# Kernel tuning notes

Measured on AMD Instinct MI355X. Metric: run time of the kernel, lower is better.

Reference implementation:

```python
import jax, jax.numpy as jnp
from jax import lax
import numpy as np

EPS = 1e-5
ALPHA = 0.2  # LeakyReLU slope


def setup_inputs() -> dict:
    key = jax.random.key(0)
    ks = jax.random.split(key, 8)
    B, N, F_IN, HID, OUT, H = 32, 512, 256, 512, 512, 4
    D = OUT // H
    return {
        "x": jax.random.normal(ks[0], (B, N, F_IN), dtype=jnp.float32),
        "adj": jax.random.uniform(ks[1], (N, N), dtype=jnp.float32),
        "gc_w": jax.random.normal(ks[2], (F_IN, HID), dtype=jnp.float32) * 0.04,
        "gc_b": jax.random.normal(ks[3], (HID,), dtype=jnp.float32) * 0.04,
        "bn1_g": jnp.ones((HID,), jnp.float32),
        "bn1_b": jnp.zeros((HID,), jnp.float32),
        "bn1_m": jnp.zeros((HID,), jnp.float32),
        "bn1_v": jnp.ones((HID,), jnp.float32),
        "gat_w": jax.random.normal(ks[4], (H, D, HID), dtype=jnp.float32) * 0.04,
        "conv_w": jax.random.normal(ks[5], (OUT, OUT, 3), dtype=jnp.float32) * 0.02,
        "conv_b": jax.random.normal(ks[6], (OUT,), dtype=jnp.float32) * 0.02,
        "bn2_g": jnp.ones((OUT,), jnp.float32),
        "bn2_b": jnp.zeros((OUT,), jnp.float32),
        "bn2_m": jnp.zeros((OUT,), jnp.float32),
        "bn2_v": jnp.ones((OUT,), jnp.float32),
    }


def reference(x, adj, gc_w, gc_b, bn1_g, bn1_b, bn1_m, bn1_v, gat_w,
              conv_w, conv_b, bn2_g, bn2_b, bn2_m, bn2_v):
    # --- GraphConvolution: adj @ (x @ W) + b ---
    support = jnp.einsum('bnc,cd->bnd', x, gc_w)
    g = jnp.einsum('nm,bmd->bnd', adj, support) + gc_b  # [B,N,HID]
    # --- BatchNorm1d over channel dim (eval mode) + ReLU ---
    g = (g - bn1_m) * (bn1_g / jnp.sqrt(bn1_v + EPS)) + bn1_b
    g = jax.nn.relu(g)
    # --- Multi-head GAT (repeat/mul/sum == attention-weighted matmul) ---
    hh = jnp.einsum('bnf,hdf->bhnd', g, gat_w)           # per-head projections
    e = jnp.einsum('bhnd,bhmd->bhnm', hh, hh)            # logits [B,H,N,N]
    e = jnp.where(e > 0, e, ALPHA * e)                   # LeakyReLU
    att = jax.nn.softmax(e, axis=-1)
    o = jnp.einsum('bhnm,bhmd->bhnd', att, hh)
    B, H, N, D = o.shape
    o = o.transpose(0, 2, 1, 3).reshape(B, N, H * D)     # concat heads [B,N,OUT]
    # --- TCN block: conv1d(k=3,pad=1) over node axis + BN(eval) + ReLU ---
    xc = o.transpose(0, 2, 1)                            # [B,C,N]
    y = lax.conv_general_dilated(xc, conv_w, (1,), ((1, 1),),
                                 dimension_numbers=('NCH', 'OIH', 'NCH'))
    y = y + conv_b[None, :, None]
    y = (y - bn2_m[None, :, None]) * (bn2_g / jnp.sqrt(bn2_v + EPS))[None, :, None] + bn2_b[None, :, None]
    y = jax.nn.relu(y)
    return y.transpose(0, 2, 1)                          # [B,N,OUT]
```

## Files before the change

kernel.cpp:

```cpp
#include <hip/hip_runtime.h>
#include <math.h>

#define BATCH 32
#define NNODE 512
#define FIN   256
#define HIDC  512
#define OUTC  512
#define NHEAD 4
#define HDIM  128
#define EPSV  1e-5f
#define ALPHA_LR 0.2f

typedef _Float16 half8 __attribute__((ext_vector_type(8)));
typedef _Float16 half4v __attribute__((ext_vector_type(4)));
typedef float floatx4 __attribute__((ext_vector_type(4)));

#define GLOBAL_TO_LDS16(g, l)                                                  \
  __builtin_amdgcn_global_load_lds(                                            \
      (const __attribute__((address_space(1))) void*)(g),                      \
      (__attribute__((address_space(3))) void*)(l), 16, 0, 0)

__device__ __forceinline__ void split_gemm_acc(
    const _Float16* __restrict__ Ah, const _Float16* __restrict__ Al, int lda,
    const _Float16* __restrict__ Bh, const _Float16* __restrict__ Bl, int ldb,
    int K, int rowBase, int colBase,
    _Float16* sAh, _Float16* sAl, _Float16* sBh, _Float16* sBl,
    floatx4 acc[4][4], int tid) {
  const int lane = tid & 63, wave = tid >> 6;
  const int wr = (wave >> 1) * 64, wc = (wave & 1) * 64;
  const int fr = lane & 15, q = lane >> 4;
  const int r = tid >> 2, ko = (tid & 3) * 8;
  for (int k0 = 0; k0 < K; k0 += 32) {
    GLOBAL_TO_LDS16(&Ah[(size_t)(rowBase + r) * lda + k0 + ko], &sAh[tid * 8]);
    GLOBAL_TO_LDS16(&Ah[(size_t)(rowBase + r + 64) * lda + k0 + ko], &sAh[2048 + tid * 8]);
    GLOBAL_TO_LDS16(&Al[(size_t)(rowBase + r) * lda + k0 + ko], &sAl[tid * 8]);
    GLOBAL_TO_LDS16(&Al[(size_t)(rowBase + r + 64) * lda + k0 + ko], &sAl[2048 + tid * 8]);
    GLOBAL_TO_LDS16(&Bh[(size_t)(colBase + r) * ldb + k0 + ko], &sBh[tid * 8]);
    GLOBAL_TO_LDS16(&Bh[(size_t)(colBase + r + 64) * ldb + k0 + ko], &sBh[2048 + tid * 8]);
    GLOBAL_TO_LDS16(&Bl[(size_t)(colBase + r) * ldb + k0 + ko], &sBl[tid * 8]);
    GLOBAL_TO_LDS16(&Bl[(size_t)(colBase + r + 64) * ldb + k0 + ko], &sBl[2048 + tid * 8]);
    __syncthreads();
    half8 ah[4], al4[4], bh[4], bl4[4];
#pragma unroll
    for (int i = 0; i < 4; ++i) {
      ah[i]  = *(const half8*)&sAh[(wr + i * 16 + fr) * 32 + q * 8];
      al4[i] = *(const half8*)&sAl[(wr + i * 16 + fr) * 32 + q * 8];
    }
#pragma unroll
    for (int j = 0; j < 4; ++j) {
      bh[j]  = *(const half8*)&sBh[(wc + j * 16 + fr) * 32 + q * 8];
      bl4[j] = *(const half8*)&sBl[(wc + j * 16 + fr) * 32 + q * 8];
    }
#pragma unroll
    for (int i = 0; i < 4; ++i)
#pragma unroll
      for (int j = 0; j < 4; ++j) {
        acc[i][j] = __builtin_amdgcn_mfma_f32_16x16x32_f16(al4[i], bh[j], acc[i][j], 0, 0, 0);
        acc[i][j] = __builtin_amdgcn_mfma_f32_16x16x32_f16(ah[i], bl4[j], acc[i][j], 0, 0, 0);
        acc[i][j] = __builtin_amdgcn_mfma_f32_16x16x32_f16(ah[i], bh[j], acc[i][j], 0, 0, 0);
      }
    __syncthreads();
  }
}

__global__ __launch_bounds__(256) void k_prep(
    const float* __restrict__ adj, const float* __restrict__ gcw,
    const float* __restrict__ gatw, const float* __restrict__ cw,
    const float* __restrict__ X,
    _Float16* __restrict__ ADJh, _Float16* __restrict__ ADJl,
    _Float16* __restrict__ GWh, _Float16* __restrict__ GWl,
    _Float16* __restrict__ GAh, _Float16* __restrict__ GAl,
    _Float16* __restrict__ WT, _Float16* __restrict__ OP,
    _Float16* __restrict__ Xh, _Float16* __restrict__ Xl) {
  const int i = blockIdx.x * 256 + threadIdx.x;
  if (i < 262144) {
    float v = adj[i];
    _Float16 h = (_Float16)v;
    ADJh[i] = h; ADJl[i] = (_Float16)(v - (float)h);
  } else if (i < 393216) {
    int j = i - 262144;
    int n = j >> 8, k = j & 255;
    float v = gcw[(size_t)k * HIDC + n];
    _Float16 h = (_Float16)v;
    GWh[j] = h; GWl[j] = (_Float16)(v - (float)h);
  } else if (i < 655360) {
    int j = i - 393216;
    float v = gatw[j];
    _Float16 h = (_Float16)v;
    GAh[j] = h; GAl[j] = (_Float16)(v - (float)h);
  } else if (i < 1441792) {
    int j = i - 655360;
    int n = j / 1536, kk = j - n * 1536;
    int tap = kk >> 9, ci = kk & 511;
    WT[j] = (_Float16)cw[(size_t)n * 1536 + ci * 3 + tap];
  } else if (i < 1474560) {
    int j = i - 1441792;
    int b = j >> 10, rs = (j >> 9) & 1, c = j & 511;
    OP[((size_t)b * 514 + rs * 513) * OUTC + c] = (_Float16)0.f;
  } else if (i < 2523136) {
    int j = (i - 1474560) * 4;
    float4 v = *(const float4*)&X[j];
    half4v h, l;
    h[0] = (_Float16)v.x; l[0] = (_Float16)(v.x - (float)h[0]);
    h[1] = (_Float16)v.y; l[1] = (_Float16)(v.y - (float)h[1]);
    h[2] = (_Float16)v.z; l[2] = (_Float16)(v.z - (float)h[2]);
    h[3] = (_Float16)v.w; l[3] = (_Float16)(v.w - (float)h[3]);
    *(half4v*)&Xh[j] = h;
    *(half4v*)&Xl[j] = l;
  }
}

__global__ __launch_bounds__(256) void k_support_t(
    const _Float16* __restrict__ GWh, const _Float16* __restrict__ GWl,
    const _Float16* __restrict__ Xh, const _Float16* __restrict__ Xl,
    _Float16* __restrict__ STh, _Float16* __restrict__ STl) {
  __shared__ _Float16 sm[4][4096];
  const int tid = threadIdx.x;
  const int rowBase = blockIdx.y * 128, colBase = blockIdx.x * 128;
  floatx4 acc[4][4] = {};
  split_gemm_acc(GWh, GWl, FIN, Xh, Xl, FIN, FIN, rowBase, colBase,
                 sm[0], sm[1], sm[2], sm[3], acc, tid);
  const int lane = tid & 63, wave = tid >> 6;
  const int wr = (wave >> 1) * 64, wc = (wave & 1) * 64;
  const int fr = lane & 15, q = lane >> 4;
#pragma unroll
  for (int i = 0; i < 4; ++i) {
    const int ch0 = rowBase + wr + i * 16 + q * 4;
#pragma unroll
    for (int rg = 0; rg < 4; ++rg) {
      size_t base = (size_t)(ch0 + rg) * 16384 + colBase + wc + fr;
#pragma unroll
      for (int j = 0; j < 4; ++j) {
        float v = acc[i][j][rg];
        _Float16 h = (_Float16)v;
        STh[base + j * 16] = h;
        STl[base + j * 16] = (_Float16)(v - (float)h);
      }
    }
  }
}

__global__ __launch_bounds__(256) void k_gcn(
    const _Float16* __restrict__ ADJh, const _Float16* __restrict__ ADJl,
    const _Float16* __restrict__ STh, const _Float16* __restrict__ STl,
    const float* __restrict__ gcb, const float* __restrict__ g1,
    const float* __restrict__ b1, const float* __restrict__ m1,
    const float* __restrict__ v1,
    _Float16* __restrict__ Gh, _Float16* __restrict__ Gl) {
  __shared__ _Float16 sm[4][4096];
  const int tid = threadIdx.x;
  const int rowBase = blockIdx.y * 128, colBase = blockIdx.x * 128;
  const int b = blockIdx.z;
  floatx4 acc[4][4] = {};
  split_gemm_acc(ADJh, ADJl, NNODE, STh + (size_t)b * NNODE, STl + (size_t)b * NNODE,
                 16384, NNODE, rowBase, colBase, sm[0], sm[1], sm[2], sm[3], acc, tid);
  const int lane = tid & 63, wave = tid >> 6;
  const int wr = (wave >> 1) * 64, wc = (wave & 1) * 64;
  const int fr = lane & 15, q = lane >> 4;
  float sc[4], of[4];
#pragma unroll
  for (int j = 0; j < 4; ++j) {
    int c = colBase + wc + j * 16 + fr;
    float s = g1[c] * rsqrtf(v1[c] + EPSV);
    sc[j] = s;
    of[j] = (gcb[c] - m1[c]) * s + b1[c];
  }
#pragma unroll
  for (int i = 0; i < 4; ++i) {
    const int n0 = rowBase + wr + i * 16 + q * 4;
#pragma unroll
    for (int rg = 0; rg < 4; ++rg) {
      size_t base = ((size_t)b * NNODE + n0 + rg) * HIDC + colBase + wc + fr;
#pragma unroll
      for (int j = 0; j < 4; ++j) {
        float v = fmaxf(fmaf(acc[i][j][rg], sc[j], of[j]), 0.0f);
        _Float16 h = (_Float16)v;
        Gh[base + j * 16] = h;
        Gl[base + j * 16] = (_Float16)(v - (float)h);
      }
    }
  }
}

__global__ __launch_bounds__(256) void k_hh(
    const _Float16* __restrict__ Gh, const _Float16* __restrict__ Gl,
    const _Float16* __restrict__ GAh, const _Float16* __restrict__ GAl,
    _Float16* __restrict__ HHh, _Float16* __restrict__ HHl) {
  __shared__ _Float16 sm[4][4096];
  const int tid = threadIdx.x;
  const int rowBase = blockIdx.y * 128, colBase = blockIdx.x * 128;
  floatx4 acc[4][4] = {};
  split_gemm_acc(Gh, Gl, HIDC, GAh, GAl, HIDC, HIDC, rowBase, colBase,
                 sm[0], sm[1], sm[2], sm[3], acc, tid);
  const int lane = tid & 63, wave = tid >> 6;
  const int wr = (wave >> 1) * 64, wc = (wave & 1) * 64;
  const int fr = lane & 15, q = lane >> 4;
#pragma unroll
  for (int i = 0; i < 4; ++i) {
    const int r0 = rowBase + wr + i * 16 + q * 4;
#pragma unroll
    for (int rg = 0; rg < 4; ++rg) {
      size_t base = (size_t)(r0 + rg) * OUTC + colBase + wc + fr;
#pragma unroll
      for (int j = 0; j < 4; ++j) {
        float v = acc[i][j][rg];
        _Float16 h = (_Float16)v;
        HHh[base + j * 16] = h;
        HHl[base + j * 16] = (_Float16)(v - (float)h);
      }
    }
  }
}

__global__ __launch_bounds__(256) void k_vt(const _Float16* __restrict__ HHh,
                                            _Float16* __restrict__ HHT) {
  __shared__ _Float16 sT[128 * 132];
  const int bt = blockIdx.x;
  const int nt = bt & 3, g = bt >> 2;
  const int bb = g >> 2, h = g & 3;
  const int tid = threadIdx.x;
  const int rr = tid >> 4, cc = (tid & 15) * 8;
#pragma unroll
  for (int it = 0; it < 8; ++it) {
    int node = rr + it * 16;
    half8 v = *(const half8*)&HHh[((size_t)bb * 512 + nt * 128 + node) * 512 + h * 128 + cc];
#pragma unroll
    for (int e = 0; e < 8; ++e) sT[(cc + e) * 132 + node] = v[e];
  }
  __syncthreads();
#pragma unroll
  for (int it = 0; it < 8; ++it) {
    int d = rr + it * 16;
    half8 v;
#pragma unroll
    for (int e = 0; e < 8; ++e) v[e] = sT[d * 132 + cc + e];
    *(half8*)&HHT[((size_t)g * 128 + d) * 512 + nt * 128 + cc] = v;
  }
}

__global__ __launch_bounds__(256, 4) void k_attn(
    const _Float16* __restrict__ HHh, const _Float16* __restrict__ HHl,
    const _Float16* __restrict__ HHT, _Float16* __restrict__ OP) {
  __shared__ _Float16 sK[8][2048];
  _Float16* sV = &sK[0][0];
  _Float16* sP = &sK[4][0];
  const int tid = threadIdx.x;
  const int lane = tid & 63, wave = tid >> 6;
  const int fr = lane & 15, q = lane >> 4;
  const int id = blockIdx.x;
  const int slot = id >> 3;
  const int g = (id & 7) + 8 * (slot >> 3);
  const int qBase = (slot & 7) * 64;
  const int bb = g >> 2, h = g & 3;
  const int w16 = wave * 16;
  const _Float16* Qh = HHh + (size_t)bb * NNODE * OUTC + h * HDIM;
  const _Float16* Ql = HHl + (size_t)bb * NNODE * OUTC + h * HDIM;
  const _Float16* VT = HHT + (size_t)g * HDIM * NNODE;
  const int rk = tid >> 2, ck = (tid & 3) * 8;

  half8 qh[4], ql[4];
#pragma unroll
  for (int k0 = 0; k0 < 4; ++k0) {
    const size_t off = (size_t)(qBase + w16 + fr) * OUTC + k0 * 32 + q * 8;
    qh[k0] = *(const half8*)&Qh[off];
    ql[k0] = *(const half8*)&Ql[off];
  }

  floatx4 oacc[8] = {};
  float m_i[4], l_i[4];
#pragma unroll
  for (int rg = 0; rg < 4; ++rg) { m_i[rg] = -1e30f; l_i[rg] = 0.f; }

  for (int kt = 0; kt < 8; ++kt) {
    const int ktb = kt * 64;
#pragma unroll
    for (int t = 0; t < 4; ++t) {
      GLOBAL_TO_LDS16(&Qh[(size_t)(ktb + rk) * OUTC + t * 32 + ck], &sK[t][tid * 8]);
      GLOBAL_TO_LDS16(&Ql[(size_t)(ktb + rk) * OUTC + t * 32 + ck], &sK[4 + t][tid * 8]);
    }
    __syncthreads();
    floatx4 sacc[4] = {};
#pragma unroll
    for (int k0 = 0; k0 < 4; ++k0)
#pragma unroll
      for (int j = 0; j < 4; ++j) {
        half8 bh = *(const half8*)&sK[k0][(j * 16 + fr) * 32 + q * 8];
        half8 bl = *(const half8*)&sK[4 + k0][(j * 16 + fr) * 32 + q * 8];
        sacc[j] = __builtin_amdgcn_mfma_f32_16x16x32_f16(ql[k0], bh, sacc[j], 0, 0, 0);
        sacc[j] = __builtin_amdgcn_mfma_f32_16x16x32_f16(qh[k0], bl, sacc[j], 0, 0, 0);
        sacc[j] = __builtin_amdgcn_mfma_f32_16x16x32_f16(qh[k0], bh, sacc[j], 0, 0, 0);
      }
    __syncthreads();
#pragma unroll
    for (int j = 0; j < 4; ++j)
#pragma unroll
      for (int rg = 0; rg < 4; ++rg) {
        float v = sacc[j][rg];
        sacc[j][rg] = v > 0.f ? v : ALPHA_LR * v;
      }
#pragma unroll
    for (int rg = 0; rg < 4; ++rg) {
      float mx = sacc[0][rg];
#pragma unroll
      for (int j = 1; j < 4; ++j) mx = fmaxf(mx, sacc[j][rg]);
      mx = fmaxf(mx, __shfl_xor(mx, 1));
      mx = fmaxf(mx, __shfl_xor(mx, 2));
      mx = fmaxf(mx, __shfl_xor(mx, 4));
      mx = fmaxf(mx, __shfl_xor(mx, 8));
      float mnew = fmaxf(m_i[rg], mx);
      float alpha = __expf(m_i[rg] - mnew);
      m_i[rg] = mnew;
      float sum = 0.f;
#pragma unroll
      for (int j = 0; j < 4; ++j) {
        float p = __expf(sacc[j][rg] - mnew);
        sacc[j][rg] = p;
        sum += p;
      }
      sum += __shfl_xor(sum, 1);
      sum += __shfl_xor(sum, 2);
      sum += __shfl_xor(sum, 4);
      sum += __shfl_xor(sum, 8);
      l_i[rg] = l_i[rg] * alpha + sum;
#pragma unroll
      for (int j = 0; j < 8; ++j) oacc[j][rg] *= alpha;
    }
#pragma unroll
    for (int l = 0; l < 4; ++l)
      GLOBAL_TO_LDS16(&VT[(size_t)((l >> 1) * 64 + rk) * NNODE + ktb + (l & 1) * 32 + ck],
                      &sV[(l & 1) * 4096 + (l >> 1) * 2048 + tid * 8]);
#pragma unroll
    for (int j = 0; j < 4; ++j)
#pragma unroll
      for (int rg = 0; rg < 4; ++rg)
        sP[(w16 + q * 4 + rg) * 68 + j * 16 + fr] = (_Float16)sacc[j][rg];
    __syncthreads();
#pragma unroll
    for (int ks = 0; ks < 2; ++ks) {
      half8 pa = *(const half8*)&sP[(w16 + fr) * 68 + ks * 32 + q * 8];
#pragma unroll
      for (int j = 0; j < 8; ++j) {
        half8 bv = *(const half8*)&sV[ks * 4096 + (j * 16 + fr) * 32 + q * 8];
        oacc[j] = __builtin_amdgcn_mfma_f32_16x16x32_f16(pa, bv, oacc[j], 0, 0, 0);
      }
    }
    __syncthreads();
  }
#pragma unroll
  for (int rg = 0; rg < 4; ++rg) {
    const float inv = 1.0f / l_i[rg];
    const int node = qBase + w16 + q * 4 + rg;
    size_t base = ((size_t)bb * 514 + 1 + node) * OUTC + h * HDIM + fr;
#pragma unroll
    for (int j = 0; j < 8; ++j)
      OP[base + j * 16] = (_Float16)(oacc[j][rg] * inv);
  }
}

__global__ __launch_bounds__(256) void k_conv_mfma(
    const _Float16* __restrict__ OP, const _Float16* __restrict__ WT,
    const float* __restrict__ cb, const float* __restrict__ g2,
    const float* __restrict__ b2, const float* __restrict__ m2,
    const float* __restrict__ v2, float* __restrict__ Y) {
  __shared__ _Float16 At[128 * 32];
  __shared__ _Float16 Bt[128 * 32];
  const int tid = threadIdx.x;
  const int lane = tid & 63, wave = tid >> 6;
  const int wr = (wave >> 1) * 64, wc = (wave & 1) * 64;
  const int id = blockIdx.y * 4 + blockIdx.x;
  const int jj = id >> 3;
  const int rowBase = ((id & 7) * 16 + (jj >> 2)) * 128;
  const int colBase = (jj & 3) * 128;
  const int b = rowBase >> 9;
  const int n0 = rowBase & 511;
  const int r = tid >> 2;
  const int ko = (tid & 3) * 8;
  floatx4 acc[4][4] = {};
  for (int k0 = 0; k0 < 3 * OUTC; k0 += 32) {
    const int tap = k0 >> 9;
    const int cib = k0 & 511;
    const size_t abase = ((size_t)b * 514 + n0 + tap) * OUTC + cib + ko;
    GLOBAL_TO_LDS16(&OP[abase + (size_t)r * OUTC],        &At[tid * 8]);
    GLOBAL_TO_LDS16(&OP[abase + (size_t)(r + 64) * OUTC], &At[2048 + tid * 8]);
    GLOBAL_TO_LDS16(&WT[(size_t)(colBase + r) * 1536 + k0 + ko],      &Bt[tid * 8]);
    GLOBAL_TO_LDS16(&WT[(size_t)(colBase + r + 64) * 1536 + k0 + ko], &Bt[2048 + tid * 8]);
    __syncthreads();
    const int fr = lane & 15, q = lane >> 4;
    half8 af[4], bf[4];
#pragma unroll
    for (int i = 0; i < 4; ++i)
      af[i] = *(const half8*)&At[(wr + i * 16 + fr) * 32 + q * 8];
#pragma unroll
    for (int j = 0; j < 4; ++j)
      bf[j] = *(const half8*)&Bt[(wc + j * 16 + fr) * 32 + q * 8];
#pragma unroll
    for (int i = 0; i < 4; ++i)
#pragma unroll
      for (int j = 0; j < 4; ++j)
        acc[i][j] = __builtin_amdgcn_mfma_f32_16x16x32_f16(af[i], bf[j], acc[i][j], 0, 0, 0);
    __syncthreads();
  }
  const int fr = lane & 15, q = lane >> 4;
  float sc[4], of[4];
#pragma unroll
  for (int j = 0; j < 4; ++j) {
    int c = colBase + wc + j * 16 + fr;
    float s = g2[c] * rsqrtf(v2[c] + EPSV);
    sc[j] = s;
    of[j] = (cb[c] - m2[c]) * s + b2[c];
  }
#pragma unroll
  for (int i = 0; i < 4; ++i) {
    const int R0r = rowBase + wr + i * 16 + q * 4;
#pragma unroll
    for (int rg = 0; rg < 4; ++rg) {
      float* dst = &Y[(size_t)(R0r + rg) * OUTC + colBase + wc + fr];
#pragma unroll
      for (int j = 0; j < 4; ++j)
        dst[j * 16] = fmaxf(fmaf(acc[i][j][rg], sc[j], of[j]), 0.0f);
    }
  }
}

extern "C" void kernel_launch(void* const* d_in, const int* in_sizes, int n_in,
                              void* d_out, int out_size, void* d_ws, size_t ws_size,
                              hipStream_t stream) {
  const float* x     = (const float*)d_in[0];
  const float* adj   = (const float*)d_in[1];
  const float* gc_w  = (const float*)d_in[2];
  const float* gc_b  = (const float*)d_in[3];
  const float* bn1_g = (const float*)d_in[4];
  const float* bn1_b = (const float*)d_in[5];
  const float* bn1_m = (const float*)d_in[6];
  const float* bn1_v = (const float*)d_in[7];
  const float* gat_w = (const float*)d_in[8];
  const float* conv_w= (const float*)d_in[9];
  const float* conv_b= (const float*)d_in[10];
  const float* bn2_g = (const float*)d_in[11];
  const float* bn2_b = (const float*)d_in[12];
  const float* bn2_m = (const float*)d_in[13];
  const float* bn2_v = (const float*)d_in[14];
  float* out = (float*)d_out;

  char* ws = (char*)d_ws;
  _Float16* STh = (_Float16*)(ws + 0);
  _Float16* STl = (_Float16*)(ws + 16777216);
  _Float16* HHh = (_Float16*)(ws + 0);
  _Float16* HHl = (_Float16*)(ws + 16777216);
  _Float16* Xh  = (_Float16*)(ws + 33554432);
  _Float16* Xl  = (_Float16*)(ws + 41943040);
  _Float16* Gh  = (_Float16*)(ws + 33554432);
  _Float16* Gl  = (_Float16*)(ws + 50331648);
  _Float16* HHT = (_Float16*)(ws + 33554432);
  _Float16* OP  = (_Float16*)(ws + 67108864);
  _Float16* WT  = (_Float16*)(ws + 83951616);
  _Float16* ADJh= (_Float16*)(ws + 85524480);
  _Float16* ADJl= (_Float16*)(ws + 86048768);
  _Float16* GWh = (_Float16*)(ws + 86573056);
  _Float16* GWl = (_Float16*)(ws + 86835200);
  _Float16* GAh = (_Float16*)(ws + 87097344);
  _Float16* GAl = (_Float16*)(ws + 87621632);

  k_prep<<<9856, 256, 0, stream>>>(adj, gc_w, gat_w, conv_w, x,
                                   ADJh, ADJl, GWh, GWl, GAh, GAl, WT, OP, Xh, Xl);
  k_support_t<<<dim3(128, 4), 256, 0, stream>>>(GWh, GWl, Xh, Xl, STh, STl);
  k_gcn<<<dim3(4, 4, 32), 256, 0, stream>>>(ADJh, ADJl, STh, STl, gc_b,
                                            bn1_g, bn1_b, bn1_m, bn1_v, Gh, Gl);
  k_hh<<<dim3(4, 128), 256, 0, stream>>>(Gh, Gl, GAh, GAl, HHh, HHl);
  k_vt<<<512, 256, 0, stream>>>(HHh, HHT);
  k_attn<<<1024, 256, 0, stream>>>(HHh, HHl, HHT, OP);
  k_conv_mfma<<<dim3(4, 128), 256, 0, stream>>>(OP, WT, conv_b,
                                                bn2_g, bn2_b, bn2_m, bn2_v, out);
}
```

Measured before the change: 303.8 us.

## Prefetch next key tile into ping-pong LDS halves during attention softmax

The attention kernel now keeps a 32KB LDS buffer split into alternating hi/lo halves plus a separate P buffer. The next key tile's high part is issued during the softmax and PV stages, overlapping it with compute, and the low part is loaded after PV into the freed half. This cuts one barrier-exposed load per iteration but raises LDS use, so launch bounds drop from 4 to 3 blocks per CU, which may lower occupancy. The V tile is also issued earlier, right after the QK stage.

```diff
diff --git a/kernel.cpp b/kernel.cpp
--- a/kernel.cpp
+++ b/kernel.cpp
@@ -238,12 +238,11 @@
   }
 }
 
-__global__ __launch_bounds__(256, 4) void k_attn(
+__global__ __launch_bounds__(256, 3) void k_attn(
     const _Float16* __restrict__ HHh, const _Float16* __restrict__ HHl,
     const _Float16* __restrict__ HHT, _Float16* __restrict__ OP) {
-  __shared__ _Float16 sK[8][2048];
-  _Float16* sV = &sK[0][0];
-  _Float16* sP = &sK[4][0];
+  __shared__ _Float16 sK[16384];
+  __shared__ _Float16 sP[64 * 68];
   const int tid = threadIdx.x;
   const int lane = tid & 63, wave = tid >> 6;
   const int fr = lane & 15, q = lane >> 4;
@@ -271,26 +270,39 @@
 #pragma unroll
   for (int rg = 0; rg < 4; ++rg) { m_i[rg] = -1e30f; l_i[rg] = 0.f; }
 
+#pragma unroll
+  for (int t = 0; t < 4; ++t) {
+    GLOBAL_TO_LDS16(&Qh[(size_t)rk * OUTC + t * 32 + ck], &sK[t * 2048 + tid * 8]);
+    GLOBAL_TO_LDS16(&Ql[(size_t)rk * OUTC + t * 32 + ck], &sK[8192 + t * 2048 + tid * 8]);
+  }
+  __syncthreads();
+
   for (int kt = 0; kt < 8; ++kt) {
     const int ktb = kt * 64;
-#pragma unroll
-    for (int t = 0; t < 4; ++t) {
-      GLOBAL_TO_LDS16(&Qh[(size_t)(ktb + rk) * OUTC + t * 32 + ck], &sK[t][tid * 8]);
-      GLOBAL_TO_LDS16(&Ql[(size_t)(ktb + rk) * OUTC + t * 32 + ck], &sK[4 + t][tid * 8]);
-    }
-    __syncthreads();
+    const int hiOff = (kt & 1) * 8192;
+    const int loOff = 8192 - hiOff;
     floatx4 sacc[4] = {};
 #pragma unroll
     for (int k0 = 0; k0 < 4; ++k0)
 #pragma unroll
       for (int j = 0; j < 4; ++j) {
-        half8 bh = *(const half8*)&sK[k0][(j * 16 + fr) * 32 + q * 8];
-        half8 bl = *(const half8*)&sK[4 + k0][(j * 16 + fr) * 32 + q * 8];
+        half8 bh = *(const half8*)&sK[hiOff + k0 * 2048 + (j * 16 + fr) * 32 + q * 8];
+        half8 bl = *(const half8*)&sK[loOff + k0 * 2048 + (j * 16 + fr) * 32 + q * 8];
         sacc[j] = __builtin_amdgcn_mfma_f32_16x16x32_f16(ql[k0], bh, sacc[j], 0, 0, 0);
         sacc[j] = __builtin_amdgcn_mfma_f32_16x16x32_f16(qh[k0], bl, sacc[j], 0, 0, 0);
         sacc[j] = __builtin_amdgcn_mfma_f32_16x16x32_f16(qh[k0], bh, sacc[j], 0, 0, 0);
       }
     __syncthreads();
+#pragma unroll
+    for (int l = 0; l < 4; ++l)
+      GLOBAL_TO_LDS16(&VT[(size_t)((l >> 1) * 64 + rk) * NNODE + ktb + (l & 1) * 32 + ck],
+                      &sK[hiOff + (l & 1) * 4096 + (l >> 1) * 2048 + tid * 8]);
+    if (kt < 7) {
+#pragma unroll
+      for (int t = 0; t < 4; ++t)
+        GLOBAL_TO_LDS16(&Qh[(size_t)(ktb + 64 + rk) * OUTC + t * 32 + ck],
+                        &sK[loOff + t * 2048 + tid * 8]);
+    }
 #pragma unroll
     for (int j = 0; j < 4; ++j)
 #pragma unroll
@@ -326,10 +338,6 @@
       for (int j = 0; j < 8; ++j) oacc[j][rg] *= alpha;
     }
 #pragma unroll
-    for (int l = 0; l < 4; ++l)
-      GLOBAL_TO_LDS16(&VT[(size_t)((l >> 1) * 64 + rk) * NNODE + ktb + (l & 1) * 32 + ck],
-                      &sV[(l & 1) * 4096 + (l >> 1) * 2048 + tid * 8]);
-#pragma unroll
     for (int j = 0; j < 4; ++j)
 #pragma unroll
       for (int rg = 0; rg < 4; ++rg)
@@ -340,11 +348,18 @@
       half8 pa = *(const half8*)&sP[(w16 + fr) * 68 + ks * 32 + q * 8];
 #pragma unroll
       for (int j = 0; j < 8; ++j) {
-        half8 bv = *(const half8*)&sV[ks * 4096 + (j * 16 + fr) * 32 + q * 8];
+        half8 bv = *(const half8*)&sK[hiOff + ks * 4096 + (j * 16 + fr) * 32 + q * 8];
         oacc[j] = __builtin_amdgcn_mfma_f32_16x16x32_f16(pa, bv, oacc[j], 0, 0, 0);
       }
     }
     __syncthreads();
+    if (kt < 7) {
+#pragma unroll
+      for (int t = 0; t < 4; ++t)
+        GLOBAL_TO_LDS16(&Ql[(size_t)(ktb + 64 + rk) * OUTC + t * 32 + ck],
+                        &sK[hiOff + t * 2048 + tid * 8]);
+      __syncthreads();
+    }
   }
 #pragma unroll
   for (int rg = 0; rg < 4; ++rg) {
```

New measurement: 300.4 us. Within noise of the previous version (-1.1%).
